# Kernel optimization log

Hardware: AMD Instinct MI355X
Metric: run time of the kernel (lower is better)

Reference implementation:

```python
import jax, jax.numpy as jnp
import numpy as np

D_MODEL = 1024
N_HEADS = 16
HEAD_DIM = D_MODEL // N_HEADS
B, S = 2, 2048


def setup_inputs() -> dict:
    key = jax.random.key(0)
    ks = jax.random.split(key, 12)
    std = 1.0 / np.sqrt(D_MODEL)
    mk = lambda k: (jax.random.normal(k, (D_MODEL, D_MODEL), jnp.float32) * std)
    return {
        "query": jax.random.normal(ks[0], (B, S, D_MODEL), jnp.float32),
        "key": jax.random.normal(ks[1], (B, S, D_MODEL), jnp.float32),
        "value": jax.random.normal(ks[2], (B, S, D_MODEL), jnp.float32),
        "Wq": mk(ks[3]), "bq": jnp.zeros((D_MODEL,), jnp.float32),
        "Wk": mk(ks[4]), "bk": jnp.zeros((D_MODEL,), jnp.float32),
        "Wv": mk(ks[5]), "bv": jnp.zeros((D_MODEL,), jnp.float32),
        "Wo": mk(ks[6]), "bo": jnp.zeros((D_MODEL,), jnp.float32),
    }


def reference(query, key, value, Wq, bq, Wk, bk, Wv, bv, Wo, bo):
    b, s, d = query.shape
    # Linear projections (torch Linear: x @ W.T + b)
    q = query @ Wq.T + bq
    k = key @ Wk.T + bk
    v = value @ Wv.T + bv
    # [B, H, S, Dh]
    split = lambda x: x.reshape(b, -1, N_HEADS, HEAD_DIM).transpose(0, 2, 1, 3)
    qh, kh, vh = split(q), split(k), split(v)
    scores = jnp.einsum("bhqd,bhkd->bhqk", qh, kh) / jnp.sqrt(
        jnp.asarray(HEAD_DIM, qh.dtype))
    attn = jax.nn.softmax(scores, axis=-1)
    out = jnp.einsum("bhqk,bhkd->bhqd", attn, vh)
    out = out.transpose(0, 2, 1, 3).reshape(b, -1, N_HEADS * HEAD_DIM)
    return out @ Wo.T + bo
```

## Files before the change

### kernel.cpp

```cpp
#include <hip/hip_runtime.h>
#include <hip/hip_bf16.h>


typedef short bf16x8 __attribute__((ext_vector_type(8)));
typedef short bf16x4 __attribute__((ext_vector_type(4)));
typedef float f32x4  __attribute__((ext_vector_type(4)));

constexpr size_t NE = (size_t)4096 * 1024;
constexpr size_t NW = (size_t)1024 * 1024;

#if __has_builtin(__builtin_amdgcn_exp2f)
#define EXP2(x) __builtin_amdgcn_exp2f(x)
#else
#define EXP2(x) exp2f(x)
#endif

__device__ __forceinline__ short f2bf(float f) {
  __hip_bfloat16 h = __float2bfloat16(f);
  return *reinterpret_cast<short*>(&h);
}

__device__ __forceinline__ void cp16(const short* g, short* l) {
  __builtin_amdgcn_global_load_lds(
      (const __attribute__((address_space(1))) void*)g,
      (__attribute__((address_space(3))) void*)l, 16, 0, 0);
}

__device__ __forceinline__ int xcd_swz(int x, int nblk) {
  return (x & 7) * (nblk >> 3) + (x >> 3);
}

__global__ __launch_bounds__(256) void cvt_kernel(
    const float* q, const float* k, const float* v,
    const float* Wq, const float* Wk, const float* Wv, const float* Wo,
    short* qb, short* kb, short* vb,
    short* Wqb, short* Wkb, short* Wvb, short* Wob) {
  const int y = blockIdx.y;
  const float* s; short* d;
  if (y < 12) {
    const int t = y >> 2;
    const size_t off = (size_t)(y & 3) << 20;
    s = (t == 0 ? q : (t == 1 ? k : v)) + off;
    d = (t == 0 ? qb : (t == 1 ? kb : vb)) + off;
  } else {
    s = (y == 12 ? Wq : (y == 13 ? Wk : (y == 14 ? Wv : Wo)));
    d = (y == 12 ? Wqb : (y == 13 ? Wkb : (y == 14 ? Wvb : Wob)));
  }
  size_t i = (size_t)blockIdx.x * 256 + threadIdx.x;
  float4 val = ((const float4*)s)[i];
  bf16x4 o;
  o[0] = f2bf(val.x); o[1] = f2bf(val.y); o[2] = f2bf(val.z); o[3] = f2bf(val.w);
  ((bf16x4*)d)[i] = o;
}

__global__ __launch_bounds__(256) void gemm_qkv(
    const short* __restrict__ A0, const short* __restrict__ A1, const short* __restrict__ A2,
    const short* __restrict__ W0, const short* __restrict__ W1, const short* __restrict__ W2,
    const float* __restrict__ b0, const float* __restrict__ b1, const float* __restrict__ b2,
    short* __restrict__ C0, short* __restrict__ C1, short* __restrict__ Cv) {
  __shared__ short As[3][128 * 32];
  __shared__ short Bs[3][128 * 32];
  const int which = blockIdx.y;
  const short* A    = which == 0 ? A0 : (which == 1 ? A1 : A2);
  const short* W    = which == 0 ? W0 : (which == 1 ? W1 : W2);
  const float* bias = which == 0 ? b0 : (which == 1 ? b1 : b2);
  const float scale = which == 0 ? 0.18033688011112042f : 1.0f;

  const int tid  = threadIdx.x;
  const int bx   = xcd_swz((int)blockIdx.x, 256);
  const int bm   = bx >> 3;
  const int bn   = bx & 7;
  const int lane = tid & 63, wid = tid >> 6;
  const int g = lane >> 4, l15 = lane & 15;
  const int wm = (wid >> 1) * 64, wn = (wid & 1) * 64;
  const int sk = (l15 >> 1) & 3;

  const int qsw = ((tid & 3) ^ ((tid >> 3) & 3)) * 8;
  const short* Ag = A + (size_t)(bm * 128 + (tid >> 2)) * 1024 + qsw;
  const short* Wg = W + (size_t)(bn * 128 + (tid >> 2)) * 1024 + qsw;
  const int wofs = wid * 512;

#define QKV_STAGE(t, b)                               \
  do {                                                \
    const int kk_ = (t) * 32;                         \
    cp16(Ag + kk_,             As[(b)] + wofs);       \
    cp16(Ag + 64 * 1024 + kk_, As[(b)] + wofs + 2048);\
    cp16(Wg + kk_,             Bs[(b)] + wofs);       \
    cp16(Wg + 64 * 1024 + kk_, Bs[(b)] + wofs + 2048);\
  } while (0)

  f32x4 acc[4][4];
#pragma unroll
  for (int i = 0; i < 4; ++i)
#pragma unroll
    for (int j = 0; j < 4; ++j) acc[i][j] = (f32x4){0.f, 0.f, 0.f, 0.f};

  QKV_STAGE(0, 0);
  QKV_STAGE(1, 1);

  for (int t = 0; t < 32; ++t) {
    const int cur = t % 3;
    if (t < 30) {
      QKV_STAGE(t + 2, (t + 2) % 3);
      asm volatile("s_waitcnt vmcnt(8)" ::: "memory");
    } else if (t == 30) {
      asm volatile("s_waitcnt vmcnt(4)" ::: "memory");
    } else {
      asm volatile("s_waitcnt vmcnt(0)" ::: "memory");
    }
    __builtin_amdgcn_s_barrier();

    bf16x8 af[4], bfr[4];
#pragma unroll
    for (int mt = 0; mt < 4; ++mt)
      af[mt] = *(const bf16x8*)&As[cur][(wm + mt * 16 + l15) * 32 + ((g ^ sk)) * 8];
#pragma unroll
    for (int nt = 0; nt < 4; ++nt)
      bfr[nt] = *(const bf16x8*)&Bs[cur][(wn + nt * 16 + l15) * 32 + ((g ^ sk)) * 8];
#pragma unroll
    for (int mt = 0; mt < 4; ++mt)
#pragma unroll
      for (int nt = 0; nt < 4; ++nt)
        acc[mt][nt] = __builtin_amdgcn_mfma_f32_16x16x32_bf16(
            af[mt], bfr[nt], acc[mt][nt], 0, 0, 0);

    asm volatile("s_waitcnt lgkmcnt(0)" ::: "memory");
    __builtin_amdgcn_s_barrier();
  }
#undef QKV_STAGE

  const int col0 = bn * 128 + wn;
  if (which < 2) {
    short* C = which == 0 ? C0 : C1;
#pragma unroll
    for (int nt = 0; nt < 4; ++nt) {
      const int col = col0 + nt * 16 + l15;
      const float bb = bias[col];
#pragma unroll
      for (int mt = 0; mt < 4; ++mt) {
        const int m0 = bm * 128 + wm + mt * 16 + g * 4;
#pragma unroll
        for (int r = 0; r < 4; ++r)
          C[(size_t)(m0 + r) * 1024 + col] = f2bf((acc[mt][nt][r] + bb) * scale);
      }
    }
  } else {
#pragma unroll
    for (int nt = 0; nt < 4; ++nt) {
      const int col = col0 + nt * 16 + l15;
      const int h = col >> 6, dh = col & 63;
      const float bb = bias[col];
#pragma unroll
      for (int mt = 0; mt < 4; ++mt) {
        const int m0 = bm * 128 + wm + mt * 16 + g * 4;
        const int bb_ = m0 >> 11, s0 = m0 & 2047;
        const int k6 = s0 & 63;
        const int cpos = (s0 & ~63) | (((k6 >> 4) & 2) << 4)
                       | (((k6 >> 2) & 3) << 3) | (((k6 >> 4) & 1) << 2);
        bf16x4 o;
#pragma unroll
        for (int r = 0; r < 4; ++r) o[r] = f2bf(acc[mt][nt][r] + bb);
        *(bf16x4*)&Cv[(((size_t)bb_ * 16 + h) * 64 + dh) * 2048 + cpos] = o;
      }
    }
  }
}

__global__ __launch_bounds__(256) void gemm_out(
    const short* __restrict__ A, const short* __restrict__ W,
    const float* __restrict__ bias, float* __restrict__ C) {
  __shared__ short As[3][64 * 32];
  __shared__ short Bs[3][128 * 32];
  const int tid  = threadIdx.x;
  const int bx   = xcd_swz((int)blockIdx.x, 512);
  const int bm   = bx >> 3;
  const int bn   = bx & 7;
  const int lane = tid & 63, wid = tid >> 6;
  const int g = lane >> 4, l15 = lane & 15;
  const int wm = (wid >> 1) * 32, wn = (wid & 1) * 64;
  const int sk = (l15 >> 1) & 3;

  const int qsw = ((tid & 3) ^ ((tid >> 3) & 3)) * 8;
  const short* Ag = A + (size_t)(bm * 64 + (tid >> 2)) * 1024 + qsw;
  const short* Wg = W + (size_t)(bn * 128 + (tid >> 2)) * 1024 + qsw;
  const int wofs = wid * 512;

#define OUT_STAGE(t, b)                               \
  do {                                                \
    const int kk_ = (t) * 32;                         \
    cp16(Ag + kk_,             As[(b)] + wofs);       \
    cp16(Wg + kk_,             Bs[(b)] + wofs);       \
    cp16(Wg + 64 * 1024 + kk_, Bs[(b)] + wofs + 2048);\
  } while (0)

  f32x4 acc[2][4];
#pragma unroll
  for (int i = 0; i < 2; ++i)
#pragma unroll
    for (int j = 0; j < 4; ++j) acc[i][j] = (f32x4){0.f, 0.f, 0.f, 0.f};

  OUT_STAGE(0, 0);
  OUT_STAGE(1, 1);

  for (int t = 0; t < 32; ++t) {
    const int cur = t % 3;
    if (t < 30) {
      OUT_STAGE(t + 2, (t + 2) % 3);
      asm volatile("s_waitcnt vmcnt(6)" ::: "memory");
    } else if (t == 30) {
      asm volatile("s_waitcnt vmcnt(3)" ::: "memory");
    } else {
      asm volatile("s_waitcnt vmcnt(0)" ::: "memory");
    }
    __builtin_amdgcn_s_barrier();

    bf16x8 af[2], bfr[4];
#pragma unroll
    for (int mt = 0; mt < 2; ++mt)
      af[mt] = *(const bf16x8*)&As[cur][(wm + mt * 16 + l15) * 32 + ((g ^ sk)) * 8];
#pragma unroll
    for (int nt = 0; nt < 4; ++nt)
      bfr[nt] = *(const bf16x8*)&Bs[cur][(wn + nt * 16 + l15) * 32 + ((g ^ sk)) * 8];
#pragma unroll
    for (int mt = 0; mt < 2; ++mt)
#pragma unroll
      for (int nt = 0; nt < 4; ++nt)
        acc[mt][nt] = __builtin_amdgcn_mfma_f32_16x16x32_bf16(
            af[mt], bfr[nt], acc[mt][nt], 0, 0, 0);

    asm volatile("s_waitcnt lgkmcnt(0)" ::: "memory");
    __builtin_amdgcn_s_barrier();
  }
#undef OUT_STAGE

  const int col0 = bn * 128 + wn;
#pragma unroll
  for (int nt = 0; nt < 4; ++nt) {
    const int col = col0 + nt * 16 + l15;
    const float bb = bias[col];
#pragma unroll
    for (int mt = 0; mt < 2; ++mt) {
      const int m0 = bm * 64 + wm + mt * 16 + g * 4;
#pragma unroll
      for (int r = 0; r < 4; ++r)
        C[(size_t)(m0 + r) * 1024 + col] = acc[mt][nt][r] + bb;
    }
  }
}

__global__ __launch_bounds__(256, 2) void attn_kernel(
    const short* __restrict__ Q, const short* __restrict__ K,
    const short* __restrict__ Vg, short* __restrict__ O) {
  __shared__ __align__(16) short KT[2][2][64 * 64];
  __shared__ __align__(16) short VT[2][2][64 * 64];

  const int tid  = threadIdx.x;
  const int bx   = xcd_swz((int)blockIdx.x, 512);
  const int qt   = bx & 15;
  const int bh   = bx >> 4;
  const int b    = bh >> 4, h = bh & 15;
  const int lane = tid & 63, wid = tid >> 6;
  const int g = lane >> 4, l15 = lane & 15;
  const int sx = l15 & 7;

  const int q0 = qt * 128 + wid * 32;
  bf16x8 qf[2][2];
#pragma unroll
  for (int mt = 0; mt < 2; ++mt) {
    const size_t base = (size_t)(b * 2048 + q0 + mt * 16 + l15) * 1024 + h * 64;
    qf[mt][0] = *(const bf16x8*)(Q + base + g * 8);
    qf[mt][1] = *(const bf16x8*)(Q + base + 32 + g * 8);
  }

  f32x4 o_acc[2][4];
#pragma unroll
  for (int i = 0; i < 2; ++i)
#pragma unroll
    for (int j = 0; j < 4; ++j) o_acc[i][j] = (f32x4){0.f, 0.f, 0.f, 0.f};
  float l_i[2] = {0.f, 0.f};

  const int lrow = lane >> 3;
  const int qc   = (lane & 7) ^ lrow;
  const int r0   = wid * 16;
  const short* KgA = K + (size_t)(b * 2048 + r0 + lrow) * 1024 + h * 64 + qc * 8;
  const short* VgA = Vg + (size_t)((b * 16 + h) * 64 + r0 + lrow) * 2048 + qc * 8;

#define ATTN_STAGE2(k2_, bf_)                                                \
  do {                                                                       \
    const int t0_ = (k2_) * 2, t1_ = t0_ + 1;                                \
    cp16(KgA + (size_t)t0_ * 64 * 1024,        &KT[bf_][0][r0 * 64]);        \
    cp16(KgA + (size_t)(t0_ * 64 + 8) * 1024,  &KT[bf_][0][(r0 + 8) * 64]);  \
    cp16(VgA + t0_ * 64,                       &VT[bf_][0][r0 * 64]);        \
    cp16(VgA + t0_ * 64 + 8 * 2048,            &VT[bf_][0][(r0 + 8) * 64]);  \
    cp16(KgA + (size_t)t1_ * 64 * 1024,        &KT[bf_][1][r0 * 64]);        \
    cp16(KgA + (size_t)(t1_ * 64 + 8) * 1024,  &KT[bf_][1][(r0 + 8) * 64]);  \
    cp16(VgA + t1_ * 64,                       &VT[bf_][1][r0 * 64]);        \
    cp16(VgA + t1_ * 64 + 8 * 2048,            &VT[bf_][1][(r0 + 8) * 64]);  \
  } while (0)

  ATTN_STAGE2(0, 0);

  for (int k2 = 0; k2 < 16; ++k2) {
    const int cur = k2 & 1;
    if (k2 < 15) {
      ATTN_STAGE2(k2 + 1, cur ^ 1);
      asm volatile("s_waitcnt vmcnt(8)" ::: "memory");
    } else {
      asm volatile("s_waitcnt vmcnt(0)" ::: "memory");
    }
    __builtin_amdgcn_s_barrier();

#pragma unroll
    for (int sub = 0; sub < 2; ++sub) {
      f32x4 sv[2][4];
#pragma unroll
      for (int nt = 0; nt < 4; ++nt) {
        const int krow = (nt * 16 + l15) * 64;
        bf16x8 kf0 = *(const bf16x8*)&KT[cur][sub][krow + ((g ^ sx) << 3)];
        bf16x8 kf1 = *(const bf16x8*)&KT[cur][sub][krow + (((g + 4) ^ sx) << 3)];
#pragma unroll
        for (int mt = 0; mt < 2; ++mt) {
          f32x4 z = (f32x4){0.f, 0.f, 0.f, 0.f};
          z = __builtin_amdgcn_mfma_f32_16x16x32_bf16(kf0, qf[mt][0], z, 0, 0, 0);
          z = __builtin_amdgcn_mfma_f32_16x16x32_bf16(kf1, qf[mt][1], z, 0, 0, 0);
          sv[mt][nt] = z;
        }
      }

      bf16x8 pf[2][2];
#pragma unroll
      for (int mt = 0; mt < 2; ++mt) {
        float s = 0.f;
#pragma unroll
        for (int nt = 0; nt < 4; ++nt)
#pragma unroll
          for (int r = 0; r < 4; ++r) {
            float p = EXP2(sv[mt][nt][r]);
            s += p;
            pf[mt][nt >> 1][(nt & 1) * 4 + r] = f2bf(p);
          }
        l_i[mt] += s;
      }

#pragma unroll
      for (int nt = 0; nt < 4; ++nt) {
        const int vrow = (nt * 16 + l15) * 64;
        bf16x8 vf0 = *(const bf16x8*)&VT[cur][sub][vrow + ((g ^ sx) << 3)];
        bf16x8 vf1 = *(const bf16x8*)&VT[cur][sub][vrow + (((g + 4) ^ sx) << 3)];
#pragma unroll
        for (int mt = 0; mt < 2; ++mt) {
          o_acc[mt][nt] = __builtin_amdgcn_mfma_f32_16x16x32_bf16(
              vf0, pf[mt][0], o_acc[mt][nt], 0, 0, 0);
          o_acc[mt][nt] = __builtin_amdgcn_mfma_f32_16x16x32_bf16(
              vf1, pf[mt][1], o_acc[mt][nt], 0, 0, 0);
        }
      }
    }

    asm volatile("s_waitcnt lgkmcnt(0)" ::: "memory");
    __builtin_amdgcn_s_barrier();
  }
#undef ATTN_STAGE2

#pragma unroll
  for (int mt = 0; mt < 2; ++mt) {
    float l = l_i[mt];
    l += __shfl_xor(l, 16, 64);
    l += __shfl_xor(l, 32, 64);
    const float inv = 1.0f / l;
    const int row = q0 + mt * 16 + l15;
    const size_t base = (size_t)(b * 2048 + row) * 1024 + h * 64;
#pragma unroll
    for (int nt = 0; nt < 4; ++nt) {
      bf16x4 o;
#pragma unroll
      for (int r = 0; r < 4; ++r) o[r] = f2bf(o_acc[mt][nt][r] * inv);
      *(bf16x4*)&O[base + nt * 16 + g * 4] = o;
    }
  }
}

extern "C" void kernel_launch(void* const* d_in, const int* in_sizes, int n_in,
                              void* d_out, int out_size, void* d_ws, size_t ws_size,
                              hipStream_t stream) {
  (void)in_sizes; (void)n_in; (void)out_size; (void)ws_size;
  const float* q  = (const float*)d_in[0];
  const float* k  = (const float*)d_in[1];
  const float* v  = (const float*)d_in[2];
  const float* Wq = (const float*)d_in[3];
  const float* bq = (const float*)d_in[4];
  const float* Wk = (const float*)d_in[5];
  const float* bk = (const float*)d_in[6];
  const float* Wv = (const float*)d_in[7];
  const float* bv = (const float*)d_in[8];
  const float* Wo = (const float*)d_in[9];
  const float* bo = (const float*)d_in[10];
  float* out = (float*)d_out;

  short* qb  = (short*)d_ws;
  short* kb  = qb + NE;
  short* vb  = kb + NE;
  short* Wqb = vb + NE;
  short* Wkb = Wqb + NW;
  short* Wvb = Wkb + NW;
  short* Wob = Wvb + NW;
  short* Qw  = Wob + NW;
  short* Kw  = Qw + NE;
  short* Vtg = Kw + NE;
  short* Ob  = qb;

  cvt_kernel<<<dim3(1024, 16), 256, 0, stream>>>(q, k, v, Wq, Wk, Wv, Wo,
                                                 qb, kb, vb, Wqb, Wkb, Wvb, Wob);
  gemm_qkv<<<dim3(256, 3), 256, 0, stream>>>(qb, kb, vb, Wqb, Wkb, Wvb,
                                             bq, bk, bv, Qw, Kw, Vtg);
  attn_kernel<<<512, 256, 0, stream>>>(Qw, Kw, Vtg, Ob);
  gemm_out<<<512, 256, 0, stream>>>(Ob, Wob, bo, out);
}
```

Baseline: 208.0 us.

## Split attention KV loop across two wave groups and merge partials via LDS

Doubles the attention block to 512 threads: two groups of four waves each process alternating 64-key tiles for the same 128 query rows, with separate double-buffered K/V LDS slices. After the loop, group 1 writes its unnormalized accumulators and row sums to LDS and group 0 adds them before normalizing and storing. This raises waves per CU and halves per-wave serial KV iterations. It also adds s_setprio around the MFMA sections. The costs are more LDS per block, which may limit how many blocks fit on a CU, and an extra reduction step through shared memory.

Result: no change. 208.5 us (+0.2%).

```diff
diff --git a/kernel.cpp b/kernel.cpp
--- a/kernel.cpp
+++ b/kernel.cpp
@@ -248,11 +248,13 @@
   }
 }
 
-__global__ __launch_bounds__(256, 2) void attn_kernel(
+__global__ __launch_bounds__(512, 4) void attn_kernel(
     const short* __restrict__ Q, const short* __restrict__ K,
     const short* __restrict__ Vg, short* __restrict__ O) {
-  __shared__ __align__(16) short KT[2][2][64 * 64];
-  __shared__ __align__(16) short VT[2][2][64 * 64];
+  __shared__ __align__(16) char smem[65536];
+  short (*KT)[2][64 * 64] = (short(*)[2][64 * 64])smem;
+  short (*VT)[2][64 * 64] = (short(*)[2][64 * 64])(smem + 32768);
+  float* M = (float*)smem;
 
   const int tid  = threadIdx.x;
   const int bx   = xcd_swz((int)blockIdx.x, 512);
@@ -260,10 +262,12 @@
   const int bh   = bx >> 4;
   const int b    = bh >> 4, h = bh & 15;
   const int lane = tid & 63, wid = tid >> 6;
+  const int par  = wid >> 2;
+  const int w4   = wid & 3;
   const int g = lane >> 4, l15 = lane & 15;
   const int sx = l15 & 7;
 
-  const int q0 = qt * 128 + wid * 32;
+  const int q0 = qt * 128 + w4 * 32;
   bf16x8 qf[2][2];
 #pragma unroll
   for (int mt = 0; mt < 2; ++mt) {
@@ -281,101 +285,119 @@
 
   const int lrow = lane >> 3;
   const int qc   = (lane & 7) ^ lrow;
-  const int r0   = wid * 16;
+  const int r0   = w4 * 16;
   const short* KgA = K + (size_t)(b * 2048 + r0 + lrow) * 1024 + h * 64 + qc * 8;
   const short* VgA = Vg + (size_t)((b * 16 + h) * 64 + r0 + lrow) * 2048 + qc * 8;
 
-#define ATTN_STAGE2(k2_, bf_)                                                \
-  do {                                                                       \
-    const int t0_ = (k2_) * 2, t1_ = t0_ + 1;                                \
-    cp16(KgA + (size_t)t0_ * 64 * 1024,        &KT[bf_][0][r0 * 64]);        \
-    cp16(KgA + (size_t)(t0_ * 64 + 8) * 1024,  &KT[bf_][0][(r0 + 8) * 64]);  \
-    cp16(VgA + t0_ * 64,                       &VT[bf_][0][r0 * 64]);        \
-    cp16(VgA + t0_ * 64 + 8 * 2048,            &VT[bf_][0][(r0 + 8) * 64]);  \
-    cp16(KgA + (size_t)t1_ * 64 * 1024,        &KT[bf_][1][r0 * 64]);        \
-    cp16(KgA + (size_t)(t1_ * 64 + 8) * 1024,  &KT[bf_][1][(r0 + 8) * 64]);  \
-    cp16(VgA + t1_ * 64,                       &VT[bf_][1][r0 * 64]);        \
-    cp16(VgA + t1_ * 64 + 8 * 2048,            &VT[bf_][1][(r0 + 8) * 64]);  \
+#define ATTN_STAGE(tk_, bf_)                                                  \
+  do {                                                                        \
+    cp16(KgA + (size_t)(tk_) * 64 * 1024,       &KT[par][bf_][r0 * 64]);      \
+    cp16(KgA + (size_t)((tk_) * 64 + 8) * 1024, &KT[par][bf_][(r0 + 8) * 64]);\
+    cp16(VgA + (tk_) * 64,                      &VT[par][bf_][r0 * 64]);      \
+    cp16(VgA + (tk_) * 64 + 8 * 2048,           &VT[par][bf_][(r0 + 8) * 64]);\
   } while (0)
 
-  ATTN_STAGE2(0, 0);
-
-  for (int k2 = 0; k2 < 16; ++k2) {
-    const int cur = k2 & 1;
-    if (k2 < 15) {
-      ATTN_STAGE2(k2 + 1, cur ^ 1);
-      asm volatile("s_waitcnt vmcnt(8)" ::: "memory");
+  ATTN_STAGE(par, 0);
+
+  for (int ktp = 0; ktp < 16; ++ktp) {
+    const int cur = ktp & 1;
+    if (ktp < 15) {
+      ATTN_STAGE(2 * (ktp + 1) + par, cur ^ 1);
+      asm volatile("s_waitcnt vmcnt(4)" ::: "memory");
     } else {
       asm volatile("s_waitcnt vmcnt(0)" ::: "memory");
     }
     __builtin_amdgcn_s_barrier();
 
-#pragma unroll
-    for (int sub = 0; sub < 2; ++sub) {
-      f32x4 sv[2][4];
+    f32x4 sv[2][4];
+    __builtin_amdgcn_s_setprio(1);
+#pragma unroll
+    for (int nt = 0; nt < 4; ++nt) {
+      const int krow = (nt * 16 + l15) * 64;
+      bf16x8 kf0 = *(const bf16x8*)&KT[par][cur][krow + ((g ^ sx) << 3)];
+      bf16x8 kf1 = *(const bf16x8*)&KT[par][cur][krow + (((g + 4) ^ sx) << 3)];
+#pragma unroll
+      for (int mt = 0; mt < 2; ++mt) {
+        f32x4 z = (f32x4){0.f, 0.f, 0.f, 0.f};
+        z = __builtin_amdgcn_mfma_f32_16x16x32_bf16(kf0, qf[mt][0], z, 0, 0, 0);
+        z = __builtin_amdgcn_mfma_f32_16x16x32_bf16(kf1, qf[mt][1], z, 0, 0, 0);
+        sv[mt][nt] = z;
+      }
+    }
+    __builtin_amdgcn_s_setprio(0);
+
+    bf16x8 pf[2][2];
+#pragma unroll
+    for (int mt = 0; mt < 2; ++mt) {
+      float s = 0.f;
+#pragma unroll
+      for (int nt = 0; nt < 4; ++nt)
+#pragma unroll
+        for (int r = 0; r < 4; ++r) {
+          float p = EXP2(sv[mt][nt][r]);
+          s += p;
+          pf[mt][nt >> 1][(nt & 1) * 4 + r] = f2bf(p);
+        }
+      l_i[mt] += s;
+    }
+
+    __builtin_amdgcn_s_setprio(1);
+#pragma unroll
+    for (int nt = 0; nt < 4; ++nt) {
+      const int vrow = (nt * 16 + l15) * 64;
+      bf16x8 vf0 = *(const bf16x8*)&VT[par][cur][vrow + ((g ^ sx) << 3)];
+      bf16x8 vf1 = *(const bf16x8*)&VT[par][cur][vrow + (((g + 4) ^ sx) << 3)];
+#pragma unroll
+      for (int mt = 0; mt < 2; ++mt) {
+        o_acc[mt][nt] = __builtin_amdgcn_mfma_f32_16x16x32_bf16(
+            vf0, pf[mt][0], o_acc[mt][nt], 0, 0, 0);
+        o_acc[mt][nt] = __builtin_amdgcn_mfma_f32_16x16x32_bf16(
+            vf1, pf[mt][1], o_acc[mt][nt], 0, 0, 0);
+      }
+    }
+    __builtin_amdgcn_s_setprio(0);
+
+    asm volatile("s_waitcnt lgkmcnt(0)" ::: "memory");
+    __builtin_amdgcn_s_barrier();
+  }
+#undef ATTN_STAGE
+
+  if (par == 1) {
+    float* dst = M + (size_t)(w4 * 64 + lane) * 36;
+#pragma unroll
+    for (int mt = 0; mt < 2; ++mt)
+#pragma unroll
+      for (int nt = 0; nt < 4; ++nt)
+        *(f32x4*)(dst + (mt * 4 + nt) * 4) = o_acc[mt][nt];
+    dst[32] = l_i[0];
+    dst[33] = l_i[1];
+  }
+  __syncthreads();
+  if (par == 0) {
+    const float* src = M + (size_t)(w4 * 64 + lane) * 36;
+#pragma unroll
+    for (int mt = 0; mt < 2; ++mt)
+#pragma unroll
+      for (int nt = 0; nt < 4; ++nt)
+        o_acc[mt][nt] += *(const f32x4*)(src + (mt * 4 + nt) * 4);
+    l_i[0] += src[32];
+    l_i[1] += src[33];
+
+#pragma unroll
+    for (int mt = 0; mt < 2; ++mt) {
+      float l = l_i[mt];
+      l += __shfl_xor(l, 16, 64);
+      l += __shfl_xor(l, 32, 64);
+      const float inv = 1.0f / l;
+      const int row = q0 + mt * 16 + l15;
+      const size_t base = (size_t)(b * 2048 + row) * 1024 + h * 64;
 #pragma unroll
       for (int nt = 0; nt < 4; ++nt) {
-        const int krow = (nt * 16 + l15) * 64;
-        bf16x8 kf0 = *(const bf16x8*)&KT[cur][sub][krow + ((g ^ sx) << 3)];
-        bf16x8 kf1 = *(const bf16x8*)&KT[cur][sub][krow + (((g + 4) ^ sx) << 3)];
-#pragma unroll
-        for (int mt = 0; mt < 2; ++mt) {
-          f32x4 z = (f32x4){0.f, 0.f, 0.f, 0.f};
-          z = __builtin_amdgcn_mfma_f32_16x16x32_bf16(kf0, qf[mt][0], z, 0, 0, 0);
-          z = __builtin_amdgcn_mfma_f32_16x16x32_bf16(kf1, qf[mt][1], z, 0, 0, 0);
-          sv[mt][nt] = z;
-        }
+        bf16x4 o;
+#pragma unroll
+        for (int r = 0; r < 4; ++r) o[r] = f2bf(o_acc[mt][nt][r] * inv);
+        *(bf16x4*)&O[base + nt * 16 + g * 4] = o;
       }
-
-      bf16x8 pf[2][2];
-#pragma unroll
-      for (int mt = 0; mt < 2; ++mt) {
-        float s = 0.f;
-#pragma unroll
-        for (int nt = 0; nt < 4; ++nt)
-#pragma unroll
-          for (int r = 0; r < 4; ++r) {
-            float p = EXP2(sv[mt][nt][r]);
-            s += p;
-            pf[mt][nt >> 1][(nt & 1) * 4 + r] = f2bf(p);
-          }
-        l_i[mt] += s;
-      }
-
-#pragma unroll
-      for (int nt = 0; nt < 4; ++nt) {
-        const int vrow = (nt * 16 + l15) * 64;
-        bf16x8 vf0 = *(const bf16x8*)&VT[cur][sub][vrow + ((g ^ sx) << 3)];
-        bf16x8 vf1 = *(const bf16x8*)&VT[cur][sub][vrow + (((g + 4) ^ sx) << 3)];
-#pragma unroll
-        for (int mt = 0; mt < 2; ++mt) {
-          o_acc[mt][nt] = __builtin_amdgcn_mfma_f32_16x16x32_bf16(
-              vf0, pf[mt][0], o_acc[mt][nt], 0, 0, 0);
-          o_acc[mt][nt] = __builtin_amdgcn_mfma_f32_16x16x32_bf16(
-              vf1, pf[mt][1], o_acc[mt][nt], 0, 0, 0);
-        }
-      }
-    }
-
-    asm volatile("s_waitcnt lgkmcnt(0)" ::: "memory");
-    __builtin_amdgcn_s_barrier();
-  }
-#undef ATTN_STAGE2
-
-#pragma unroll
-  for (int mt = 0; mt < 2; ++mt) {
-    float l = l_i[mt];
-    l += __shfl_xor(l, 16, 64);
-    l += __shfl_xor(l, 32, 64);
-    const float inv = 1.0f / l;
-    const int row = q0 + mt * 16 + l15;
-    const size_t base = (size_t)(b * 2048 + row) * 1024 + h * 64;
-#pragma unroll
-    for (int nt = 0; nt < 4; ++nt) {
-      bf16x4 o;
-#pragma unroll
-      for (int r = 0; r < 4; ++r) o[r] = f2bf(o_acc[mt][nt][r] * inv);
-      *(bf16x4*)&O[base + nt * 16 + g * 4] = o;
     }
   }
 }
@@ -413,6 +435,6 @@
                                                  qb, kb, vb, Wqb, Wkb, Wvb, Wob);
   gemm_qkv<<<dim3(256, 3), 256, 0, stream>>>(qb, kb, vb, Wqb, Wkb, Wvb,
                                              bq, bk, bv, Qw, Kw, Vtg);
-  attn_kernel<<<512, 256, 0, stream>>>(Qw, Kw, Vtg, Ob);
+  attn_kernel<<<512, 512, 0, stream>>>(Qw, Kw, Vtg, Ob);
   gemm_out<<<512, 256, 0, stream>>>(Ob, Wob, bo, out);
 }
```
